# Kernel optimization log

Hardware: AMD Instinct MI355X
Metric: run time of the kernel (lower is better)

The kernel has to match this reference:

```python
import jax, jax.numpy as jnp
import numpy as np

B, N, H, S, NSEC = 1, 8192, 256, 128, 8
TAU = 0.5
DEPTH_LO, DEPTH_HI = 0.0, 2.4
PADDING = 0.1
EPS = 1e-6
_p = float(np.clip(TAU, 1e-4, 1.0 - 1e-4))
LOGIT_TAU = float(np.log(_p / (1.0 - _p)))


def mlp(p, W1, b1, W2, b2, W3, b3, W4, b4):
    # p: [..., 3] -> logit [...]
    h = jax.nn.softplus(p @ W1 + b1)
    h = jax.nn.softplus(h @ W2 + b2)
    h = jax.nn.softplus(h @ W3 + b3)
    return (h @ W4 + b4)[..., 0]


def cube_intersection(ray0, rd):
    # Faithful port of check_ray_intersection_with_unit_cube.
    p_dist = 0.5 + PADDING / 2.0
    plane = jnp.concatenate([jnp.full((3,), p_dist), jnp.full((3,), -p_dist)])  # (6,)
    nom = plane - jnp.tile(ray0, (1, 1, 2))          # (B,N,6)
    den = jnp.tile(rd, (1, 1, 2))
    den = jnp.where(jnp.abs(den) < 1e-9, 1e-9, den)  # numerical guard
    d_int = nom / den                                 # (B,N,6)
    p_int = ray0[:, :, None, :] + d_int[..., None] * rd[:, :, None, :]  # (B,N,6,3)
    inside = jnp.all(jnp.abs(p_int) <= p_dist + EPS, axis=-1)           # (B,N,6)
    mask = inside.sum(-1) == 2                                           # rays hitting cube
    # pick the (exactly two) intersecting planes in ascending plane order,
    # matching torch boolean indexing semantics
    plane_id = jnp.arange(6)
    key = jnp.where(inside, plane_id, plane_id + 6)
    idx2 = jnp.argsort(key, axis=-1)[..., :2]                            # (B,N,2)
    p2 = jnp.take_along_axis(p_int, idx2[..., None], axis=2)            # (B,N,2,3)
    norm_rd = jnp.linalg.norm(rd, axis=-1)                               # (B,N)
    d2 = jnp.linalg.norm(p2 - ray0[:, :, None, :], axis=-1) / norm_rd[..., None]
    d2 = jnp.where(mask[..., None], d2, 0.0)
    d2 = jnp.sort(d2, axis=-1)
    return d2, mask


def _secant(d_low, f_low, d_high, f_high):
    den = f_high - f_low
    den = jnp.where(jnp.abs(den) < 1e-12, 1e-12, den)
    return -f_low * (d_high - d_low) / den + d_low


def reference(ray0, ray_direction, W1, b1, W2, b2, W3, b3, W4, b4):
    rd = ray_direction
    dec = lambda p: mlp(p, W1, b1, W2, b2, W3, b3, W4, b4)
    sg = jax.lax.stop_gradient

    # ---- proposal depths (no grad, as torch no_grad ray-marching) ----
    t = jnp.linspace(0.0, 1.0, S)                       # (S,)
    d_default = DEPTH_LO + t * (DEPTH_HI - DEPTH_LO)
    d2, mask_cube = cube_intersection(ray0, rd)
    d_cube = d2[..., 0:1] + t * (d2[..., 1:2] - d2[..., 0:1])   # (B,N,S)
    d_prop = jnp.where(mask_cube[..., None], d_cube, d_default)
    d_prop = sg(d_prop)

    p_prop = sg(ray0)[:, :, None, :] + d_prop[..., None] * sg(rd)[:, :, None, :]
    val = sg(dec(p_prop)) - LOGIT_TAU                   # (B,N,S)

    mask_0_not_occupied = val[..., 0] < 0
    sign_matrix = jnp.concatenate(
        [jnp.sign(val[..., :-1] * val[..., 1:]), jnp.ones(val.shape[:-1] + (1,), val.dtype)], -1)
    cost = sign_matrix * jnp.arange(S, 0, -1, dtype=val.dtype)
    idx = jnp.argmin(cost, -1)                          # first sign-change step
    vmin = jnp.min(cost, -1)
    f_low = jnp.take_along_axis(val, idx[..., None], -1)[..., 0]
    mask = (vmin < 0) & (f_low < 0) & mask_0_not_occupied

    idx_hi = jnp.minimum(idx + 1, S - 1)
    d_low = jnp.take_along_axis(d_prop, idx[..., None], -1)[..., 0]
    d_high = jnp.take_along_axis(d_prop, idx_hi[..., None], -1)[..., 0]
    f_high = jnp.take_along_axis(val, idx_hi[..., None], -1)[..., 0]

    # ---- secant refinement (no grad in torch) ----
    r0s, rds = sg(ray0), sg(rd)
    d_pred = _secant(d_low, f_low, d_high, f_high)
    for _ in range(NSEC):
        f_mid = sg(dec(r0s + d_pred[..., None] * rds)) - LOGIT_TAU
        low = f_mid < 0
        d_low = jnp.where(low, d_pred, d_low)
        f_low = jnp.where(low, f_mid, f_low)
        d_high = jnp.where(low, d_high, d_pred)
        f_high = jnp.where(low, f_high, f_mid)
        d_pred = _secant(d_low, f_low, d_high, f_high)

    # ---- differentiable implicit-gradient correction (analytic backward of
    # DepthFunction: dd/dtheta = -(df/dtheta)/(df/dd) at the surface point) ----
    d_star = sg(d_pred)
    f_of_d = lambda d: dec(ray0 + d[..., None] * rd) - LOGIT_TAU
    f_val = f_of_d(d_star)                              # differentiable wrt params/rays
    _, df_dd = jax.jvp(f_of_d, (d_star,), (jnp.ones_like(d_star),))
    df_dd = sg(df_dd)
    df_dd = jnp.where(jnp.abs(df_dd) < 1e-6,
                      jnp.where(df_dd < 0, -1e-6, 1e-6), df_dd)
    d_out = d_star - f_val / df_dd
    d_final = jnp.where(mask, d_out, 0.0)
    return d_final


def setup_inputs() -> dict:
    key = jax.random.key(0)
    ks = jax.random.split(key, 10)
    origin = jnp.array([0.0, 0.0, -1.5])
    ray0 = origin + 0.01 * jax.random.normal(ks[0], (B, N, 3), dtype=jnp.float32)
    target = jax.random.uniform(ks[1], (B, N, 3), minval=-0.4, maxval=0.4, dtype=jnp.float32)
    rd = target - ray0
    rd = rd / jnp.linalg.norm(rd, axis=-1, keepdims=True)
    W1 = jax.random.normal(ks[2], (3, H), dtype=jnp.float32) / jnp.sqrt(3.0)
    b1 = 0.1 * jax.random.normal(ks[3], (H,), dtype=jnp.float32)
    W2 = jax.random.normal(ks[4], (H, H), dtype=jnp.float32) / jnp.sqrt(float(H))
    b2 = 0.1 * jax.random.normal(ks[5], (H,), dtype=jnp.float32)
    W3 = jax.random.normal(ks[6], (H, H), dtype=jnp.float32) / jnp.sqrt(float(H))
    b3 = 0.1 * jax.random.normal(ks[7], (H,), dtype=jnp.float32)
    W4 = jax.random.normal(ks[8], (H, 1), dtype=jnp.float32) / jnp.sqrt(float(H))
    b4 = 0.1 * jax.random.normal(ks[9], (1,), dtype=jnp.float32)
    return {"ray0": ray0, "ray_direction": rd, "W1": W1, "b1": b1,
            "W2": W2, "b2": b2, "W3": W3, "b3": b3, "W4": W4, "b4": b4}
```

## Files before the change

kernel.cpp:

```cpp
#include <hip/hip_runtime.h>
#include <math.h>

#define NRAY 8192
#define SSAMP 128
#define HD 256
#define AROW 264
#define A1ROW 40
#define FIXCAP 262144
#define FIXTHR 0.025f

typedef short s16x8 __attribute__((ext_vector_type(8)));
typedef float f32x4 __attribute__((ext_vector_type(4)));

__device__ __forceinline__ unsigned short f2bf(float f) {
    unsigned u = __float_as_uint(f);
    u += 0x7fffu + ((u >> 16) & 1u);
    return (unsigned short)(u >> 16);
}
__device__ __forceinline__ unsigned short f2bf_t(float f) {
    return (unsigned short)(__float_as_uint(f) >> 16);
}
__device__ __forceinline__ float bf2f(unsigned short s) {
    return __uint_as_float(((unsigned)s) << 16);
}
__device__ __forceinline__ void split2(float f, unsigned short& hi, unsigned short& lo) {
    unsigned u = __float_as_uint(f);
    hi = (unsigned short)(u >> 16);
    float r = f - __uint_as_float(u & 0xFFFF0000u);
    lo = f2bf(r);
}
__device__ __forceinline__ float softplus_fast(float x) {
    return fmaxf(x, 0.0f) + __logf(1.0f + __expf(-fabsf(x)));
}
__device__ __forceinline__ float softplus_cheap(float x) {
    float m = __expf(-fabsf(x));
    float p = fmaf(m, fmaf(0.14258f, m, -0.44943f), 1.0f);
    return fmaxf(x, 0.0f) + m * p;
}
__device__ __forceinline__ float sigmoid_fast(float x) {
    return 1.0f / (1.0f + __expf(-x));
}

__global__ __launch_bounds__(256)
void prep_kernel(const float* __restrict__ W1, const float* __restrict__ b1,
                 const float* __restrict__ W2, const float* __restrict__ W3,
                 const float* __restrict__ ray0, const float* __restrict__ rdg,
                 unsigned short* __restrict__ P2, unsigned short* __restrict__ P3,
                 unsigned short* __restrict__ B1, float* __restrict__ rayinfo,
                 int* __restrict__ fix_cnt) {
    const int b = blockIdx.x, tid = threadIdx.x;
    if (b < 256) {
        int idx = b * 256 + tid;
        int k = idx >> 8, n = idx & 255;
        int nt = n >> 4, kt = k >> 5, lq = (k >> 3) & 3, j = k & 7;
        int lane = (lq << 4) | (n & 15);
        size_t off = (size_t)((nt * 8 + kt) * 2) * 512 + (size_t)lane * 8 + j;
        float w = W2[idx];
        unsigned short hi = f2bf(w);
        P2[off] = hi; P2[off + 512] = f2bf(w - bf2f(hi));
        w = W3[idx];
        hi = f2bf(w);
        P3[off] = hi; P3[off + 512] = f2bf(w - bf2f(hi));
    } else if (b < 288) {
        int idx = (b - 256) * 256 + tid;
        int w = idx & 511;
        int lane = w >> 3, j = w & 7;
        int k = ((lane >> 4) << 3) + j;
        int n = ((idx >> 9) << 4) + (lane & 15);
        unsigned short s = 0;
        if (k < 3) s = f2bf(W1[k * HD + n]);
        else if (k == 3) s = f2bf(b1[n]);
        else if (k < 7) s = f2bf(W1[(k - 4) * HD + n]);
        else if (k == 7) { unsigned short bh = f2bf(b1[n]); s = f2bf(b1[n] - bf2f(bh)); }
        else if (k < 11) { float wv = W1[(k - 8) * HD + n]; unsigned short wh = f2bf(wv); s = f2bf(wv - bf2f(wh)); }
        B1[idx] = s;
    } else {
        int r = (b - 288) * 256 + tid;
        if (r == 0) *fix_cnt = 0;
        float o0 = ray0[3 * r], o1 = ray0[3 * r + 1], o2 = ray0[3 * r + 2];
        float v0 = rdg[3 * r], v1 = rdg[3 * r + 1], v2 = rdg[3 * r + 2];
        const float pd = 0.55f, lim = pd + 1e-6f;
        float di[6]; int insk[6]; int cnt = 0;
        for (int k = 0; k < 6; k++) {
            int a = k % 3;
            float pl = (k < 3) ? pd : -pd;
            float den = (a == 0) ? v0 : ((a == 1) ? v1 : v2);
            if (fabsf(den) < 1e-9f) den = 1e-9f;
            float oa = (a == 0) ? o0 : ((a == 1) ? o1 : o2);
            float dd = (pl - oa) / den;
            float px = o0 + dd * v0, py = o1 + dd * v1, pz = o2 + dd * v2;
            int ins = (fabsf(px) <= lim) && (fabsf(py) <= lim) && (fabsf(pz) <= lim);
            di[k] = dd; insk[k] = ins; cnt += ins;
        }
        float d0 = 0.f, sl = 2.4f;
        if (cnt == 2) {
            int k1 = -1, k2 = -1;
            for (int k = 0; k < 6; k++) if (insk[k]) { if (k1 < 0) k1 = k; else k2 = k; }
            float nrd = sqrtf(v0 * v0 + v1 * v1 + v2 * v2);
            float ax = di[k1] * v0, ay = di[k1] * v1, az = di[k1] * v2;
            float d1n = sqrtf(ax * ax + ay * ay + az * az) / nrd;
            float bx = di[k2] * v0, by = di[k2] * v1, bz = di[k2] * v2;
            float d2n = sqrtf(bx * bx + by * by + bz * bz) / nrd;
            d0 = fminf(d1n, d2n);
            sl = fmaxf(d1n, d2n) - d0;
        }
        float* ri = rayinfo + (size_t)r * 8;
        ri[0] = d0; ri[1] = sl;
        ri[2] = o0; ri[3] = o1; ri[4] = o2;
        ri[5] = v0; ri[6] = v1; ri[7] = v2;
    }
}

template<int MT>
__device__ __forceinline__ void gemm_l1(const unsigned short* A1,
                                        const unsigned short* __restrict__ B1,
                                        f32x4 acc[MT][4], int lane, int ntbase) {
    const int r15 = lane & 15, q = lane >> 4;
    s16x8 bh[4];
#pragma unroll
    for (int nt = 0; nt < 4; nt++)
        bh[nt] = *(((const s16x8*)B1) + (size_t)(ntbase + nt) * 64 + lane);
#pragma unroll
    for (int mt = 0; mt < MT; mt++) {
        s16x8 ah = *(const s16x8*)(A1 + (mt * 16 + r15) * A1ROW + q * 8);
#pragma unroll
        for (int nt = 0; nt < 4; nt++)
            acc[mt][nt] = __builtin_amdgcn_mfma_f32_16x16x32_bf16(ah, bh[nt], (f32x4){0.f,0.f,0.f,0.f}, 0, 0, 0);
    }
}

template<int MT>
__device__ __forceinline__ void gemm_1t(const unsigned short* Ahi,
                                        const unsigned short* __restrict__ Bp,
                                        f32x4 acc[MT][4], int lane, int ntbase) {
#pragma unroll
    for (int mt = 0; mt < MT; mt++)
#pragma unroll
        for (int nt = 0; nt < 4; nt++) acc[mt][nt] = (f32x4){0.f, 0.f, 0.f, 0.f};
    const int r15 = lane & 15, q = lane >> 4;
#pragma unroll 2
    for (int kt = 0; kt < 8; kt++) {
        s16x8 bh[4];
#pragma unroll
        for (int nt = 0; nt < 4; nt++) {
            const s16x8* bp = ((const s16x8*)Bp) + (size_t)((ntbase + nt) * 8 + kt) * 128 + lane;
            bh[nt] = bp[0];
        }
        const int kc = kt * 32 + q * 8;
#pragma unroll
        for (int mt = 0; mt < MT; mt++) {
            s16x8 ah = *(const s16x8*)(Ahi + (mt * 16 + r15) * AROW + kc);
#pragma unroll
            for (int nt = 0; nt < 4; nt++)
                acc[mt][nt] = __builtin_amdgcn_mfma_f32_16x16x32_bf16(ah, bh[nt], acc[mt][nt], 0, 0, 0);
        }
    }
}

template<int MT>
__device__ __forceinline__ void gemm_3t(const unsigned short* Ahi, const unsigned short* Alo,
                                        const unsigned short* __restrict__ Bp,
                                        f32x4 acc[MT][4], int lane, int ntbase) {
#pragma unroll
    for (int mt = 0; mt < MT; mt++)
#pragma unroll
        for (int nt = 0; nt < 4; nt++) acc[mt][nt] = (f32x4){0.f, 0.f, 0.f, 0.f};
    const int r15 = lane & 15, q = lane >> 4;
#pragma unroll 2
    for (int kt = 0; kt < 8; kt++) {
        s16x8 bh[4], bl[4];
#pragma unroll
        for (int nt = 0; nt < 4; nt++) {
            const s16x8* bp = ((const s16x8*)Bp) + (size_t)((ntbase + nt) * 8 + kt) * 128 + lane;
            bh[nt] = bp[0];
            bl[nt] = bp[64];
        }
        const int kc = kt * 32 + q * 8;
#pragma unroll
        for (int mt = 0; mt < MT; mt++) {
            s16x8 ah = *(const s16x8*)(Ahi + (mt * 16 + r15) * AROW + kc);
            s16x8 al = *(const s16x8*)(Alo + (mt * 16 + r15) * AROW + kc);
#pragma unroll
            for (int nt = 0; nt < 4; nt++) {
                acc[mt][nt] = __builtin_amdgcn_mfma_f32_16x16x32_bf16(ah, bh[nt], acc[mt][nt], 0, 0, 0);
                acc[mt][nt] = __builtin_amdgcn_mfma_f32_16x16x32_bf16(ah, bl[nt], acc[mt][nt], 0, 0, 0);
                acc[mt][nt] = __builtin_amdgcn_mfma_f32_16x16x32_bf16(al, bh[nt], acc[mt][nt], 0, 0, 0);
            }
        }
    }
}

template<int MT>
__device__ __forceinline__ void gemm_dual(const unsigned short* Avh, const unsigned short* Avl,
                                          const unsigned short* Ath, const unsigned short* Atl,
                                          const unsigned short* __restrict__ Bp,
                                          f32x4 av[MT][4], f32x4 at[MT][4], int lane, int ntbase) {
#pragma unroll
    for (int mt = 0; mt < MT; mt++)
#pragma unroll
        for (int nt = 0; nt < 4; nt++) {
            av[mt][nt] = (f32x4){0.f, 0.f, 0.f, 0.f};
            at[mt][nt] = (f32x4){0.f, 0.f, 0.f, 0.f};
        }
    const int r15 = lane & 15, q = lane >> 4;
#pragma unroll 2
    for (int kt = 0; kt < 8; kt++) {
        s16x8 bh[4], bl[4];
#pragma unroll
        for (int nt = 0; nt < 4; nt++) {
            const s16x8* bp = ((const s16x8*)Bp) + (size_t)((ntbase + nt) * 8 + kt) * 128 + lane;
            bh[nt] = bp[0];
            bl[nt] = bp[64];
        }
        const int kc = kt * 32 + q * 8;
#pragma unroll
        for (int mt = 0; mt < MT; mt++) {
            s16x8 avh = *(const s16x8*)(Avh + (mt * 16 + r15) * AROW + kc);
            s16x8 avl = *(const s16x8*)(Avl + (mt * 16 + r15) * AROW + kc);
            s16x8 ath = *(const s16x8*)(Ath + (mt * 16 + r15) * AROW + kc);
            s16x8 atl = *(const s16x8*)(Atl + (mt * 16 + r15) * AROW + kc);
#pragma unroll
            for (int nt = 0; nt < 4; nt++) {
                av[mt][nt] = __builtin_amdgcn_mfma_f32_16x16x32_bf16(avh, bh[nt], av[mt][nt], 0, 0, 0);
                av[mt][nt] = __builtin_amdgcn_mfma_f32_16x16x32_bf16(avh, bl[nt], av[mt][nt], 0, 0, 0);
                av[mt][nt] = __builtin_amdgcn_mfma_f32_16x16x32_bf16(avl, bh[nt], av[mt][nt], 0, 0, 0);
                at[mt][nt] = __builtin_amdgcn_mfma_f32_16x16x32_bf16(ath, bh[nt], at[mt][nt], 0, 0, 0);
                at[mt][nt] = __builtin_amdgcn_mfma_f32_16x16x32_bf16(ath, bl[nt], at[mt][nt], 0, 0, 0);
                at[mt][nt] = __builtin_amdgcn_mfma_f32_16x16x32_bf16(atl, bh[nt], at[mt][nt], 0, 0, 0);
            }
        }
    }
}

template<int MT>
__device__ __forceinline__ void epi_l1(f32x4 acc[MT][4], unsigned short* Ahi, int lane, int wn0) {
    const int r15 = lane & 15, q = lane >> 4;
#pragma unroll
    for (int mt = 0; mt < MT; mt++)
#pragma unroll
        for (int nt = 0; nt < 4; nt++) {
            int col = wn0 + nt * 16 + r15;
#pragma unroll
            for (int reg = 0; reg < 4; reg++) {
                int row = mt * 16 + q * 4 + reg;
                Ahi[row * AROW + col] = f2bf_t(softplus_cheap(acc[mt][nt][reg]));
            }
        }
}

template<int MT>
__device__ __forceinline__ void epi_l1_sp(f32x4 acc[MT][4], unsigned short* Ahi, unsigned short* Alo,
                                          int lane, int wn0) {
    const int r15 = lane & 15, q = lane >> 4;
#pragma unroll
    for (int mt = 0; mt < MT; mt++)
#pragma unroll
        for (int nt = 0; nt < 4; nt++) {
            int col = wn0 + nt * 16 + r15;
#pragma unroll
            for (int reg = 0; reg < 4; reg++) {
                int row = mt * 16 + q * 4 + reg;
                float h = softplus_fast(acc[mt][nt][reg]);
                unsigned short hi, lo;
                split2(h, hi, lo);
                Ahi[row * AROW + col] = hi;
                Alo[row * AROW + col] = lo;
            }
        }
}

template<int MT>
__device__ __forceinline__ void epi_hidden_1t(f32x4 acc[MT][4], const float* __restrict__ b,
                                              unsigned short* Ahi, int lane, int wn0) {
    const int r15 = lane & 15, q = lane >> 4;
#pragma unroll
    for (int mt = 0; mt < MT; mt++)
#pragma unroll
        for (int nt = 0; nt < 4; nt++) {
            int col = wn0 + nt * 16 + r15;
            float bb = b[col];
#pragma unroll
            for (int reg = 0; reg < 4; reg++) {
                int row = mt * 16 + q * 4 + reg;
                Ahi[row * AROW + col] = f2bf_t(softplus_cheap(acc[mt][nt][reg] + bb));
            }
        }
}

template<int MT>
__device__ __forceinline__ void epi_hidden_sp(f32x4 acc[MT][4], const float* __restrict__ b,
                                              unsigned short* Ahi, unsigned short* Alo,
                                              int lane, int wn0) {
    const int r15 = lane & 15, q = lane >> 4;
#pragma unroll
    for (int mt = 0; mt < MT; mt++)
#pragma unroll
        for (int nt = 0; nt < 4; nt++) {
            int col = wn0 + nt * 16 + r15;
            float bb = b[col];
#pragma unroll
            for (int reg = 0; reg < 4; reg++) {
                int row = mt * 16 + q * 4 + reg;
                float h = softplus_fast(acc[mt][nt][reg] + bb);
                unsigned short hi, lo;
                split2(h, hi, lo);
                Ahi[row * AROW + col] = hi;
                Alo[row * AROW + col] = lo;
            }
        }
}

template<int MT>
__device__ __forceinline__ void epi_dual(f32x4 av[MT][4], f32x4 at[MT][4], const float* __restrict__ b,
                                         unsigned short* Avh, unsigned short* Avl,
                                         unsigned short* Ath, unsigned short* Atl,
                                         int lane, int wn0) {
    const int r15 = lane & 15, q = lane >> 4;
#pragma unroll
    for (int mt = 0; mt < MT; mt++)
#pragma unroll
        for (int nt = 0; nt < 4; nt++) {
            int col = wn0 + nt * 16 + r15;
            float bb = b[col];
#pragma unroll
            for (int reg = 0; reg < 4; reg++) {
                int row = mt * 16 + q * 4 + reg;
                float z = av[mt][nt][reg] + bb;
                float h = softplus_fast(z);
                float ht = sigmoid_fast(z) * at[mt][nt][reg];
                unsigned short hi, lo;
                split2(h, hi, lo);
                Avh[row * AROW + col] = hi;
                Avl[row * AROW + col] = lo;
                split2(ht, hi, lo);
                Ath[row * AROW + col] = hi;
                Atl[row * AROW + col] = lo;
            }
        }
}

template<int MT, bool CH>
__device__ __forceinline__ void l4_reduce(f32x4 acc[MT][4], const float* __restrict__ b3,
                                          const float* __restrict__ W4,
                                          float* partial, int lane, int wn0) {
    const int r15 = lane & 15, q = lane >> 4;
    float w4v[4], b3v[4];
#pragma unroll
    for (int nt = 0; nt < 4; nt++) {
        int col = wn0 + nt * 16 + r15;
        w4v[nt] = W4[col]; b3v[nt] = b3[col];
    }
#pragma unroll
    for (int mt = 0; mt < MT; mt++)
#pragma unroll
        for (int reg = 0; reg < 4; reg++) {
            float p = 0.f;
#pragma unroll
            for (int nt = 0; nt < 4; nt++) {
                float z = acc[mt][nt][reg] + b3v[nt];
                float h = CH ? softplus_cheap(z) : softplus_fast(z);
                p += h * w4v[nt];
            }
#pragma unroll
            for (int m = 1; m < 16; m <<= 1) p += __shfl_xor(p, m, 64);
            if (r15 == 0) partial[mt * 16 + q * 4 + reg] = p;
        }
}

template<int MT>
__device__ __forceinline__ void l4_reduce_dual(f32x4 av[MT][4], f32x4 at[MT][4],
                                               const float* __restrict__ b3, const float* __restrict__ W4,
                                               float* pv, float* pt, int lane, int wn0) {
    const int r15 = lane & 15, q = lane >> 4;
    float w4v[4], b3v[4];
#pragma unroll
    for (int nt = 0; nt < 4; nt++) {
        int col = wn0 + nt * 16 + r15;
        w4v[nt] = W4[col]; b3v[nt] = b3[col];
    }
#pragma unroll
    for (int mt = 0; mt < MT; mt++)
#pragma unroll
        for (int reg = 0; reg < 4; reg++) {
            float sv = 0.f, st = 0.f;
#pragma unroll
            for (int nt = 0; nt < 4; nt++) {
                float z = av[mt][nt][reg] + b3v[nt];
                sv += softplus_fast(z) * w4v[nt];
                st += sigmoid_fast(z) * at[mt][nt][reg] * w4v[nt];
            }
#pragma unroll
            for (int m = 1; m < 16; m <<= 1) {
                sv += __shfl_xor(sv, m, 64);
                st += __shfl_xor(st, m, 64);
            }
            if (r15 == 0) {
                pv[mt * 16 + q * 4 + reg] = sv;
                pt[mt * 16 + q * 4 + reg] = st;
            }
        }
}

__global__ __launch_bounds__(256, 4)
void coarse_mfma(const float* __restrict__ rayinfo,
                 const unsigned short* __restrict__ B1,
                 const unsigned short* __restrict__ P2, const float* __restrict__ b2,
                 const unsigned short* __restrict__ P3, const float* __restrict__ b3,
                 const float* __restrict__ W4, const float* __restrict__ b4,
                 float* __restrict__ val_out, float* __restrict__ dprop_out,
                 int* __restrict__ fix_cnt, int* __restrict__ fix_list) {
    __shared__ __align__(16) unsigned short Ahi[64 * AROW];
    __shared__ __align__(16) unsigned short A1[64 * A1ROW];
    float* partial = (float*)A1;
    const int tid = threadIdx.x;
    const int lane = tid & 63, wave = tid >> 6;
    const int r = blockIdx.x >> 1, half = blockIdx.x & 1;

    if (tid < 64) {
        const float* ri = rayinfo + (size_t)r * 8;
        const int s = half * 64 + tid;
        float t = (float)s * (1.0f / 127.0f);
        float d = fmaf(t, ri[1], ri[0]);
        dprop_out[r * SSAMP + s] = d;
        float px = fmaf(d, ri[5], ri[2]);
        float py = fmaf(d, ri[6], ri[3]);
        float pz = fmaf(d, ri[7], ri[4]);
        unsigned short hx, lx, hy, ly, hz, lz;
        split2(px, hx, lx); split2(py, hy, ly); split2(pz, hz, lz);
        unsigned short* row = A1 + tid * A1ROW;
        row[0] = hx; row[1] = hy; row[2] = hz; row[3] = 0x3F80u;
        row[4] = lx; row[5] = ly; row[6] = lz; row[7] = 0x3F80u;
        row[8] = hx; row[9] = hy; row[10] = hz;
#pragma unroll
        for (int c = 11; c < 32; c++) row[c] = 0;
    }
    __syncthreads();
    f32x4 acc[4][4];
    gemm_l1<4>(A1, B1, acc, lane, wave * 4);
    epi_l1<4>(acc, Ahi, lane, wave * 64);
    __syncthreads();
    gemm_1t<4>(Ahi, P2, acc, lane, wave * 4);
    __syncthreads();
    epi_hidden_1t<4>(acc, b2, Ahi, lane, wave * 64);
    __syncthreads();
    gemm_1t<4>(Ahi, P3, acc, lane, wave * 4);
    l4_reduce<4, true>(acc, b3, W4, &partial[wave * 64], lane, wave * 64);
    __syncthreads();
    if (tid < 64) {
        float v = partial[tid] + partial[64 + tid] + partial[128 + tid] + partial[192 + tid] + b4[0];
        int idx = r * SSAMP + half * 64 + tid;
        val_out[idx] = v;
        if (fabsf(v) < FIXTHR) {
            int pos = atomicAdd(fix_cnt, 1);
            if (pos < FIXCAP) fix_list[pos] = idx;
        }
    }
}

__global__ __launch_bounds__(256, 2)
void fixup3_mfma(const int* __restrict__ counter, const int* __restrict__ list,
                 float* __restrict__ val, const float* __restrict__ dprop,
                 const float* __restrict__ ray0, const float* __restrict__ rdg,
                 const unsigned short* __restrict__ B1,
                 const unsigned short* __restrict__ P2, const float* __restrict__ b2,
                 const unsigned short* __restrict__ P3, const float* __restrict__ b3,
                 const float* __restrict__ W4, const float* __restrict__ b4) {
    __shared__ __align__(16) unsigned short Ahi[64 * AROW];
    __shared__ __align__(16) unsigned short Alo[64 * AROW];
    __shared__ __align__(16) unsigned short A1[64 * A1ROW];
    __shared__ float partial[4][64];
    __shared__ int bidxs[64];
    const int cnt = min(*counter, FIXCAP);
    const int base = blockIdx.x * 64;
    if (base >= cnt) return;
    const int tid = threadIdx.x;
    const int lane = tid & 63, wave = tid >> 6;
    if (tid < 64) {
        const int i = min(base + tid, cnt - 1);
        const int bidx = list[i];
        bidxs[tid] = bidx;
        const int rr = bidx >> 7;
        float d = dprop[bidx];
        float px = ray0[3 * rr] + d * rdg[3 * rr];
        float py = ray0[3 * rr + 1] + d * rdg[3 * rr + 1];
        float pz = ray0[3 * rr + 2] + d * rdg[3 * rr + 2];
        unsigned short hx, lx, hy, ly, hz, lz;
        split2(px, hx, lx); split2(py, hy, ly); split2(pz, hz, lz);
        unsigned short* row = A1 + tid * A1ROW;
        row[0] = hx; row[1] = hy; row[2] = hz; row[3] = 0x3F80u;
        row[4] = lx; row[5] = ly; row[6] = lz; row[7] = 0x3F80u;
        row[8] = hx; row[9] = hy; row[10] = hz;
#pragma unroll
        for (int c = 11; c < 32; c++) row[c] = 0;
    }
    __syncthreads();
    f32x4 acc[4][4];
    gemm_l1<4>(A1, B1, acc, lane, wave * 4);
    epi_l1_sp<4>(acc, Ahi, Alo, lane, wave * 64);
    __syncthreads();
    gemm_3t<4>(Ahi, Alo, P2, acc, lane, wave * 4);
    __syncthreads();
    epi_hidden_sp<4>(acc, b2, Ahi, Alo, lane, wave * 64);
    __syncthreads();
    gemm_3t<4>(Ahi, Alo, P3, acc, lane, wave * 4);
    l4_reduce<4, false>(acc, b3, W4, &partial[wave][0], lane, wave * 64);
    __syncthreads();
    if (tid < 64) {
        float v = partial[0][tid] + partial[1][tid] + partial[2][tid] + partial[3][tid] + b4[0];
        val[bidxs[tid]] = v;
    }
}

__global__ __launch_bounds__(256, 4)
void refine_mfma(const float* __restrict__ val, const float* __restrict__ dprop,
                 const float* __restrict__ ray0, const float* __restrict__ rdg,
                 const float* __restrict__ W1, const float* __restrict__ b1,
                 const unsigned short* __restrict__ P2, const float* __restrict__ b2,
                 const unsigned short* __restrict__ P3, const float* __restrict__ b3,
                 const float* __restrict__ W4, const float* __restrict__ b4,
                 float* __restrict__ out) {
    __shared__ __align__(16) unsigned short Avh[16 * AROW];
    __shared__ __align__(16) unsigned short Avl[16 * AROW];
    __shared__ __align__(16) unsigned short Ath[16 * AROW];
    __shared__ __align__(16) unsigned short Atl[16 * AROW];
    __shared__ float partial[4][16], ptan[4][16];
    __shared__ float dl[16], fl[16], dh[16], fh[16], dps[16];
    __shared__ int mks[16];
    unsigned short* Ahi = Avh;
    const int tid = threadIdx.x;
    const int lane = tid & 63, wave = tid >> 6;
    const int r0 = blockIdx.x * 16;

    for (int i = 0; i < 4; i++) {
        const int r = r0 + wave * 4 + i;
        const float2 v = *(const float2*)(val + (size_t)r * SSAMP + lane * 2);
        const float2 dd = *(const float2*)(dprop + (size_t)r * SSAMP + lane * 2);
        float vnext = __shfl_down(v.x, 1, 64);
        const int s0 = lane * 2, s1 = s0 + 1;
        float pr0 = v.x * v.y;
        int sg0 = (pr0 > 0.f) ? 1 : ((pr0 < 0.f) ? -1 : 0);
        int k0 = (sg0 * (SSAMP - s0) + 129) * 256 + s0;
        int k1;
        if (lane == 63) {
            k1 = (1 + 129) * 256 + 127;
        } else {
            float pr1 = v.y * vnext;
            int sg1 = (pr1 > 0.f) ? 1 : ((pr1 < 0.f) ? -1 : 0);
            k1 = (sg1 * (SSAMP - s1) + 129) * 256 + s1;
        }
        int k = min(k0, k1);
#pragma unroll
        for (int m = 1; m < 64; m <<= 1) k = min(k, __shfl_xor(k, m, 64));
        int bidx = k & 255;
        int cmin = (k >> 8) - 129;
        int idxh = min(bidx + 1, SSAMP - 1);
        int ow = bidx >> 1, oh = idxh >> 1;
        float fa = __shfl(v.x, ow, 64), fb = __shfl(v.y, ow, 64);
        float da = __shfl(dd.x, ow, 64), db = __shfl(dd.y, ow, 64);
        float fa2 = __shfl(v.x, oh, 64), fb2 = __shfl(v.y, oh, 64);
        float da2 = __shfl(dd.x, oh, 64), db2 = __shfl(dd.y, oh, 64);
        float v0 = __shfl(v.x, 0, 64);
        if (lane == 0) {
            float f_low = (bidx & 1) ? fb : fa;
            float d_low = (bidx & 1) ? db : da;
            float f_high = (idxh & 1) ? fb2 : fa2;
            float d_high = (idxh & 1) ? db2 : da2;
            int sl = wave * 4 + i;
            mks[sl] = (cmin < 0) && (f_low < 0.f) && (v0 < 0.f);
            float den = f_high - f_low;
            if (fabsf(den) < 1e-12f) den = 1e-12f;
            dl[sl] = d_low; fl[sl] = f_low; dh[sl] = d_high; fh[sl] = f_high;
            dps[sl] = -f_low * (d_high - d_low) / den + d_low;
        }
    }
    __syncthreads();
    for (int it = 0; it < 8; it++) {
        {
            const int pt = tid >> 4, jb = (tid & 15) << 4;
            const int rr = r0 + pt;
            float d = dps[pt];
            float px = ray0[3 * rr] + d * rdg[3 * rr];
            float py = ray0[3 * rr + 1] + d * rdg[3 * rr + 1];
            float pz = ray0[3 * rr + 2] + d * rdg[3 * rr + 2];
            for (int j = jb; j < jb + 16; j += 4) {
                float4 wa = *(const float4*)(W1 + j);
                float4 wb = *(const float4*)(W1 + 256 + j);
                float4 wc = *(const float4*)(W1 + 512 + j);
                float4 bb = *(const float4*)(b1 + j);
                float z[4];
                z[0] = fmaf(px, wa.x, fmaf(py, wb.x, fmaf(pz, wc.x, bb.x)));
                z[1] = fmaf(px, wa.y, fmaf(py, wb.y, fmaf(pz, wc.y, bb.y)));
                z[2] = fmaf(px, wa.z, fmaf(py, wb.z, fmaf(pz, wc.z, bb.z)));
                z[3] = fmaf(px, wa.w, fmaf(py, wb.w, fmaf(pz, wc.w, bb.w)));
#pragma unroll
                for (int i = 0; i < 4; i++)
                    Ahi[pt * AROW + j + i] = f2bf_t(softplus_cheap(z[i]));
            }
        }
        __syncthreads();
        f32x4 acc[1][4];
        gemm_1t<1>(Ahi, P2, acc, lane, wave * 4);
        __syncthreads();
        epi_hidden_1t<1>(acc, b2, Ahi, lane, wave * 64);
        __syncthreads();
        gemm_1t<1>(Ahi, P3, acc, lane, wave * 4);
        l4_reduce<1, true>(acc, b3, W4, &partial[wave][0], lane, wave * 64);
        __syncthreads();
        if (tid < 16) {
            float fm = partial[0][tid] + partial[1][tid] + partial[2][tid] + partial[3][tid] + b4[0];
            float dpv = dps[tid];
            float dlv = dl[tid], flv = fl[tid], dhv = dh[tid], fhv = fh[tid];
            if (fm < 0.f) { dlv = dpv; flv = fm; } else { dhv = dpv; fhv = fm; }
            float den = fhv - flv;
            if (fabsf(den) < 1e-12f) den = 1e-12f;
            dps[tid] = -flv * (dhv - dlv) / den + dlv;
            dl[tid] = dlv; fl[tid] = flv; dh[tid] = dhv; fh[tid] = fhv;
        }
        __syncthreads();
    }
    {
        const int pt = tid >> 4, jb = (tid & 15) << 4;
        const int rr = r0 + pt;
        float d = dps[pt];
        float v0 = rdg[3 * rr], v1 = rdg[3 * rr + 1], v2 = rdg[3 * rr + 2];
        float px = ray0[3 * rr] + d * v0;
        float py = ray0[3 * rr + 1] + d * v1;
        float pz = ray0[3 * rr + 2] + d * v2;
        for (int j = jb; j < jb + 16; j += 4) {
            float4 wa = *(const float4*)(W1 + j);
            float4 wb = *(const float4*)(W1 + 256 + j);
            float4 wc = *(const float4*)(W1 + 512 + j);
            float4 bb = *(const float4*)(b1 + j);
            float z[4], zt[4];
            z[0] = fmaf(px, wa.x, fmaf(py, wb.x, fmaf(pz, wc.x, bb.x)));
            z[1] = fmaf(px, wa.y, fmaf(py, wb.y, fmaf(pz, wc.y, bb.y)));
            z[2] = fmaf(px, wa.z, fmaf(py, wb.z, fmaf(pz, wc.z, bb.z)));
            z[3] = fmaf(px, wa.w, fmaf(py, wb.w, fmaf(pz, wc.w, bb.w)));
            zt[0] = fmaf(v0, wa.x, fmaf(v1, wb.x, v2 * wc.x));
            zt[1] = fmaf(v0, wa.y, fmaf(v1, wb.y, v2 * wc.y));
            zt[2] = fmaf(v0, wa.z, fmaf(v1, wb.z, v2 * wc.z));
            zt[3] = fmaf(v0, wa.w, fmaf(v1, wb.w, v2 * wc.w));
#pragma unroll
            for (int i = 0; i < 4; i++) {
                float h = softplus_fast(z[i]);
                float ht = sigmoid_fast(z[i]) * zt[i];
                unsigned short hi, lo;
                split2(h, hi, lo);
                Avh[pt * AROW + j + i] = hi;
                Avl[pt * AROW + j + i] = lo;
                split2(ht, hi, lo);
                Ath[pt * AROW + j + i] = hi;
                Atl[pt * AROW + j + i] = lo;
            }
        }
    }
    __syncthreads();
    f32x4 av[1][4], at[1][4];
    gemm_dual<1>(Avh, Avl, Ath, Atl, P2, av, at, lane, wave * 4);
    __syncthreads();
    epi_dual<1>(av, at, b2, Avh, Avl, Ath, Atl, lane, wave * 64);
    __syncthreads();
    gemm_dual<1>(Avh, Avl, Ath, Atl, P3, av, at, lane, wave * 4);
    l4_reduce_dual<1>(av, at, b3, W4, &partial[wave][0], &ptan[wave][0], lane, wave * 64);
    __syncthreads();
    if (tid < 16) {
        float f = partial[0][tid] + partial[1][tid] + partial[2][tid] + partial[3][tid] + b4[0];
        float ft = ptan[0][tid] + ptan[1][tid] + ptan[2][tid] + ptan[3][tid];
        if (fabsf(ft) < 1e-6f) ft = (ft < 0.f) ? -1e-6f : 1e-6f;
        float dres = dps[tid] - f / ft;
        out[r0 + tid] = mks[tid] ? dres : 0.0f;
    }
}

extern "C" void kernel_launch(void* const* d_in, const int* in_sizes, int n_in,
                              void* d_out, int out_size, void* d_ws, size_t ws_size,
                              hipStream_t stream) {
    const float* ray0 = (const float*)d_in[0];
    const float* rdg  = (const float*)d_in[1];
    const float* W1 = (const float*)d_in[2];
    const float* b1 = (const float*)d_in[3];
    const float* W2 = (const float*)d_in[4];
    const float* b2 = (const float*)d_in[5];
    const float* W3 = (const float*)d_in[6];
    const float* b3 = (const float*)d_in[7];
    const float* W4 = (const float*)d_in[8];
    const float* b4 = (const float*)d_in[9];
    float* out = (float*)d_out;

    float* ws = (float*)d_ws;
    float* val    = ws;
    float* dprop  = ws + (size_t)SSAMP * NRAY;
    unsigned short* P2 = (unsigned short*)(ws + (size_t)2 * SSAMP * NRAY);
    unsigned short* P3 = P2 + 131072;
    unsigned short* B1 = P3 + 131072;
    float* rayinfo = (float*)(B1 + 8192);
    int* fix_cnt  = (int*)(rayinfo + (size_t)NRAY * 8);
    int* fix_list = fix_cnt + 64;

    hipLaunchKernelGGL(prep_kernel, dim3(320), dim3(256), 0, stream,
                       W1, b1, W2, W3, ray0, rdg, P2, P3, B1, rayinfo, fix_cnt);
    hipLaunchKernelGGL(coarse_mfma, dim3(NRAY * 2), dim3(256), 0, stream,
                       rayinfo, B1, P2, b2, P3, b3, W4, b4, val, dprop, fix_cnt, fix_list);
    hipLaunchKernelGGL(fixup3_mfma, dim3(FIXCAP / 64), dim3(256), 0, stream,
                       fix_cnt, fix_list, val, dprop, ray0, rdg,
                       B1, P2, b2, P3, b3, W4, b4);
    hipLaunchKernelGGL(refine_mfma, dim3(NRAY / 16), dim3(256), 0, stream,
                       val, dprop, ray0, rdg, W1, b1, P2, b2, P3, b3, W4, b4, out);
}
```

Before: 718.2 us.

## Split refine kernel into 8-ray, 2-wave blocks with wider per-wave N tiles

The refine kernel now handles 8 rays per block with 128 threads instead of 16 rays with 256 threads, which doubles the grid size. Each of the two waves covers 8 output n-tiles, using new gemm, epilogue and reduce helpers sized for 8 tiles. The MFMA M dimension is still 16, so rows 8-15 of the shared tangent and value buffers are zeroed and half of each MFMA does no useful work. The aim is more blocks in flight to hide latency in this small, serial secant/Newton stage, paid for with wasted matrix work and more B-fragment register pressure.

```diff
diff --git a/kernel.cpp b/kernel.cpp
--- a/kernel.cpp
+++ b/kernel.cpp
@@ -191,48 +191,6 @@
 }
 
 template<int MT>
-__device__ __forceinline__ void gemm_dual(const unsigned short* Avh, const unsigned short* Avl,
-                                          const unsigned short* Ath, const unsigned short* Atl,
-                                          const unsigned short* __restrict__ Bp,
-                                          f32x4 av[MT][4], f32x4 at[MT][4], int lane, int ntbase) {
-#pragma unroll
-    for (int mt = 0; mt < MT; mt++)
-#pragma unroll
-        for (int nt = 0; nt < 4; nt++) {
-            av[mt][nt] = (f32x4){0.f, 0.f, 0.f, 0.f};
-            at[mt][nt] = (f32x4){0.f, 0.f, 0.f, 0.f};
-        }
-    const int r15 = lane & 15, q = lane >> 4;
-#pragma unroll 2
-    for (int kt = 0; kt < 8; kt++) {
-        s16x8 bh[4], bl[4];
-#pragma unroll
-        for (int nt = 0; nt < 4; nt++) {
-            const s16x8* bp = ((const s16x8*)Bp) + (size_t)((ntbase + nt) * 8 + kt) * 128 + lane;
-            bh[nt] = bp[0];
-            bl[nt] = bp[64];
-        }
-        const int kc = kt * 32 + q * 8;
-#pragma unroll
-        for (int mt = 0; mt < MT; mt++) {
-            s16x8 avh = *(const s16x8*)(Avh + (mt * 16 + r15) * AROW + kc);
-            s16x8 avl = *(const s16x8*)(Avl + (mt * 16 + r15) * AROW + kc);
-            s16x8 ath = *(const s16x8*)(Ath + (mt * 16 + r15) * AROW + kc);
-            s16x8 atl = *(const s16x8*)(Atl + (mt * 16 + r15) * AROW + kc);
-#pragma unroll
-            for (int nt = 0; nt < 4; nt++) {
-                av[mt][nt] = __builtin_amdgcn_mfma_f32_16x16x32_bf16(avh, bh[nt], av[mt][nt], 0, 0, 0);
-                av[mt][nt] = __builtin_amdgcn_mfma_f32_16x16x32_bf16(avh, bl[nt], av[mt][nt], 0, 0, 0);
-                av[mt][nt] = __builtin_amdgcn_mfma_f32_16x16x32_bf16(avl, bh[nt], av[mt][nt], 0, 0, 0);
-                at[mt][nt] = __builtin_amdgcn_mfma_f32_16x16x32_bf16(ath, bh[nt], at[mt][nt], 0, 0, 0);
-                at[mt][nt] = __builtin_amdgcn_mfma_f32_16x16x32_bf16(ath, bl[nt], at[mt][nt], 0, 0, 0);
-                at[mt][nt] = __builtin_amdgcn_mfma_f32_16x16x32_bf16(atl, bh[nt], at[mt][nt], 0, 0, 0);
-            }
-        }
-    }
-}
-
-template<int MT>
 __device__ __forceinline__ void epi_l1(f32x4 acc[MT][4], unsigned short* Ahi, int lane, int wn0) {
     const int r15 = lane & 15, q = lane >> 4;
 #pragma unroll
@@ -310,35 +268,6 @@
         }
 }
 
-template<int MT>
-__device__ __forceinline__ void epi_dual(f32x4 av[MT][4], f32x4 at[MT][4], const float* __restrict__ b,
-                                         unsigned short* Avh, unsigned short* Avl,
-                                         unsigned short* Ath, unsigned short* Atl,
-                                         int lane, int wn0) {
-    const int r15 = lane & 15, q = lane >> 4;
-#pragma unroll
-    for (int mt = 0; mt < MT; mt++)
-#pragma unroll
-        for (int nt = 0; nt < 4; nt++) {
-            int col = wn0 + nt * 16 + r15;
-            float bb = b[col];
-#pragma unroll
-            for (int reg = 0; reg < 4; reg++) {
-                int row = mt * 16 + q * 4 + reg;
-                float z = av[mt][nt][reg] + bb;
-                float h = softplus_fast(z);
-                float ht = sigmoid_fast(z) * at[mt][nt][reg];
-                unsigned short hi, lo;
-                split2(h, hi, lo);
-                Avh[row * AROW + col] = hi;
-                Avl[row * AROW + col] = lo;
-                split2(ht, hi, lo);
-                Ath[row * AROW + col] = hi;
-                Atl[row * AROW + col] = lo;
-            }
-        }
-}
-
 template<int MT, bool CH>
 __device__ __forceinline__ void l4_reduce(f32x4 acc[MT][4], const float* __restrict__ b3,
                                           const float* __restrict__ W4,
@@ -367,38 +296,153 @@
         }
 }
 
-template<int MT>
-__device__ __forceinline__ void l4_reduce_dual(f32x4 av[MT][4], f32x4 at[MT][4],
-                                               const float* __restrict__ b3, const float* __restrict__ W4,
-                                               float* pv, float* pt, int lane, int wn0) {
-    const int r15 = lane & 15, q = lane >> 4;
-    float w4v[4], b3v[4];
-#pragma unroll
-    for (int nt = 0; nt < 4; nt++) {
+__device__ __forceinline__ void gemm_1t8(const unsigned short* Ahi,
+                                         const unsigned short* __restrict__ Bp,
+                                         f32x4 acc[8], int lane, int ntbase) {
+#pragma unroll
+    for (int nt = 0; nt < 8; nt++) acc[nt] = (f32x4){0.f, 0.f, 0.f, 0.f};
+    const int r15 = lane & 15, q = lane >> 4;
+#pragma unroll 2
+    for (int kt = 0; kt < 8; kt++) {
+        s16x8 bh[8];
+#pragma unroll
+        for (int nt = 0; nt < 8; nt++)
+            bh[nt] = *(((const s16x8*)Bp) + (size_t)((ntbase + nt) * 8 + kt) * 128 + lane);
+        const int kc = kt * 32 + q * 8;
+        s16x8 ah = *(const s16x8*)(Ahi + r15 * AROW + kc);
+#pragma unroll
+        for (int nt = 0; nt < 8; nt++)
+            acc[nt] = __builtin_amdgcn_mfma_f32_16x16x32_bf16(ah, bh[nt], acc[nt], 0, 0, 0);
+    }
+}
+
+__device__ __forceinline__ void gemm_dual8(const unsigned short* Avh, const unsigned short* Avl,
+                                           const unsigned short* Ath, const unsigned short* Atl,
+                                           const unsigned short* __restrict__ Bp,
+                                           f32x4 av[8], f32x4 at[8], int lane, int ntbase) {
+#pragma unroll
+    for (int nt = 0; nt < 8; nt++) {
+        av[nt] = (f32x4){0.f, 0.f, 0.f, 0.f};
+        at[nt] = (f32x4){0.f, 0.f, 0.f, 0.f};
+    }
+    const int r15 = lane & 15, q = lane >> 4;
+    for (int kt = 0; kt < 8; kt++) {
+        const int kc = kt * 32 + q * 8;
+        s16x8 avh = *(const s16x8*)(Avh + r15 * AROW + kc);
+        s16x8 avl = *(const s16x8*)(Avl + r15 * AROW + kc);
+        s16x8 ath = *(const s16x8*)(Ath + r15 * AROW + kc);
+        s16x8 atl = *(const s16x8*)(Atl + r15 * AROW + kc);
+#pragma unroll
+        for (int nt = 0; nt < 8; nt++) {
+            const s16x8* bp = ((const s16x8*)Bp) + (size_t)((ntbase + nt) * 8 + kt) * 128 + lane;
+            s16x8 bh = bp[0];
+            s16x8 bl = bp[64];
+            av[nt] = __builtin_amdgcn_mfma_f32_16x16x32_bf16(avh, bh, av[nt], 0, 0, 0);
+            av[nt] = __builtin_amdgcn_mfma_f32_16x16x32_bf16(avh, bl, av[nt], 0, 0, 0);
+            av[nt] = __builtin_amdgcn_mfma_f32_16x16x32_bf16(avl, bh, av[nt], 0, 0, 0);
+            at[nt] = __builtin_amdgcn_mfma_f32_16x16x32_bf16(ath, bh, at[nt], 0, 0, 0);
+            at[nt] = __builtin_amdgcn_mfma_f32_16x16x32_bf16(ath, bl, at[nt], 0, 0, 0);
+            at[nt] = __builtin_amdgcn_mfma_f32_16x16x32_bf16(atl, bh, at[nt], 0, 0, 0);
+        }
+    }
+}
+
+__device__ __forceinline__ void epi_hidden8(f32x4 acc[8], const float* __restrict__ b,
+                                            unsigned short* Ahi, int lane, int wn0) {
+    const int r15 = lane & 15, q = lane >> 4;
+#pragma unroll
+    for (int nt = 0; nt < 8; nt++) {
+        int col = wn0 + nt * 16 + r15;
+        float bb = b[col];
+#pragma unroll
+        for (int reg = 0; reg < 4; reg++) {
+            int row = q * 4 + reg;
+            Ahi[row * AROW + col] = f2bf_t(softplus_cheap(acc[nt][reg] + bb));
+        }
+    }
+}
+
+__device__ __forceinline__ void epi_dual8(f32x4 av[8], f32x4 at[8], const float* __restrict__ b,
+                                          unsigned short* Avh, unsigned short* Avl,
+                                          unsigned short* Ath, unsigned short* Atl,
+                                          int lane, int wn0) {
+    const int r15 = lane & 15, q = lane >> 4;
+#pragma unroll
+    for (int nt = 0; nt < 8; nt++) {
+        int col = wn0 + nt * 16 + r15;
+        float bb = b[col];
+#pragma unroll
+        for (int reg = 0; reg < 4; reg++) {
+            int row = q * 4 + reg;
+            float z = av[nt][reg] + bb;
+            float h = softplus_fast(z);
+            float ht = sigmoid_fast(z) * at[nt][reg];
+            unsigned short hi, lo;
+            split2(h, hi, lo);
+            Avh[row * AROW + col] = hi;
+            Avl[row * AROW + col] = lo;
+            split2(ht, hi, lo);
+            Ath[row * AROW + col] = hi;
+            Atl[row * AROW + col] = lo;
+        }
+    }
+}
+
+template<bool CH>
+__device__ __forceinline__ void l4_reduce8(f32x4 acc[8], const float* __restrict__ b3,
+                                           const float* __restrict__ W4,
+                                           float* partial, int lane, int wn0) {
+    const int r15 = lane & 15, q = lane >> 4;
+    float w4v[8], b3v[8];
+#pragma unroll
+    for (int nt = 0; nt < 8; nt++) {
         int col = wn0 + nt * 16 + r15;
         w4v[nt] = W4[col]; b3v[nt] = b3[col];
     }
 #pragma unroll
-    for (int mt = 0; mt < MT; mt++)
-#pragma unroll
-        for (int reg = 0; reg < 4; reg++) {
-            float sv = 0.f, st = 0.f;
-#pragma unroll
-            for (int nt = 0; nt < 4; nt++) {
-                float z = av[mt][nt][reg] + b3v[nt];
-                sv += softplus_fast(z) * w4v[nt];
-                st += sigmoid_fast(z) * at[mt][nt][reg] * w4v[nt];
-            }
-#pragma unroll
-            for (int m = 1; m < 16; m <<= 1) {
-                sv += __shfl_xor(sv, m, 64);
-                st += __shfl_xor(st, m, 64);
-            }
-            if (r15 == 0) {
-                pv[mt * 16 + q * 4 + reg] = sv;
-                pt[mt * 16 + q * 4 + reg] = st;
-            }
-        }
+    for (int reg = 0; reg < 4; reg++) {
+        float p = 0.f;
+#pragma unroll
+        for (int nt = 0; nt < 8; nt++) {
+            float z = acc[nt][reg] + b3v[nt];
+            float h = CH ? softplus_cheap(z) : softplus_fast(z);
+            p += h * w4v[nt];
+        }
+#pragma unroll
+        for (int m = 1; m < 16; m <<= 1) p += __shfl_xor(p, m, 64);
+        if (r15 == 0) partial[q * 4 + reg] = p;
+    }
+}
+
+__device__ __forceinline__ void l4_reduce_dual8(f32x4 av[8], f32x4 at[8],
+                                                const float* __restrict__ b3, const float* __restrict__ W4,
+                                                float* pv, float* pt, int lane, int wn0) {
+    const int r15 = lane & 15, q = lane >> 4;
+    float w4v[8], b3v[8];
+#pragma unroll
+    for (int nt = 0; nt < 8; nt++) {
+        int col = wn0 + nt * 16 + r15;
+        w4v[nt] = W4[col]; b3v[nt] = b3[col];
+    }
+#pragma unroll
+    for (int reg = 0; reg < 4; reg++) {
+        float sv = 0.f, st = 0.f;
+#pragma unroll
+        for (int nt = 0; nt < 8; nt++) {
+            float z = av[nt][reg] + b3v[nt];
+            sv += softplus_fast(z) * w4v[nt];
+            st += sigmoid_fast(z) * at[nt][reg] * w4v[nt];
+        }
+#pragma unroll
+        for (int m = 1; m < 16; m <<= 1) {
+            sv += __shfl_xor(sv, m, 64);
+            st += __shfl_xor(st, m, 64);
+        }
+        if (r15 == 0) {
+            pv[q * 4 + reg] = sv;
+            pt[q * 4 + reg] = st;
+        }
+    }
 }
 
 __global__ __launch_bounds__(256, 4)
@@ -511,7 +555,7 @@
     }
 }
 
-__global__ __launch_bounds__(256, 4)
+__global__ __launch_bounds__(128, 2)
 void refine_mfma(const float* __restrict__ val, const float* __restrict__ dprop,
                  const float* __restrict__ ray0, const float* __restrict__ rdg,
                  const float* __restrict__ W1, const float* __restrict__ b1,
@@ -523,13 +567,13 @@
     __shared__ __align__(16) unsigned short Avl[16 * AROW];
     __shared__ __align__(16) unsigned short Ath[16 * AROW];
     __shared__ __align__(16) unsigned short Atl[16 * AROW];
-    __shared__ float partial[4][16], ptan[4][16];
-    __shared__ float dl[16], fl[16], dh[16], fh[16], dps[16];
-    __shared__ int mks[16];
+    __shared__ float partial[2][16], ptan[2][16];
+    __shared__ float dl[8], fl[8], dh[8], fh[8], dps[8];
+    __shared__ int mks[8];
     unsigned short* Ahi = Avh;
     const int tid = threadIdx.x;
     const int lane = tid & 63, wave = tid >> 6;
-    const int r0 = blockIdx.x * 16;
+    const int r0 = blockIdx.x * 8;
 
     for (int i = 0; i < 4; i++) {
         const int r = r0 + wave * 4 + i;
@@ -598,16 +642,16 @@
             }
         }
         __syncthreads();
-        f32x4 acc[1][4];
-        gemm_1t<1>(Ahi, P2, acc, lane, wave * 4);
+        f32x4 acc[8];
+        gemm_1t8(Ahi, P2, acc, lane, wave * 8);
         __syncthreads();
-        epi_hidden_1t<1>(acc, b2, Ahi, lane, wave * 64);
+        epi_hidden8(acc, b2, Ahi, lane, wave * 128);
         __syncthreads();
-        gemm_1t<1>(Ahi, P3, acc, lane, wave * 4);
-        l4_reduce<1, true>(acc, b3, W4, &partial[wave][0], lane, wave * 64);
+        gemm_1t8(Ahi, P3, acc, lane, wave * 8);
+        l4_reduce8<true>(acc, b3, W4, &partial[wave][0], lane, wave * 128);
         __syncthreads();
-        if (tid < 16) {
-            float fm = partial[0][tid] + partial[1][tid] + partial[2][tid] + partial[3][tid] + b4[0];
+        if (tid < 8) {
+            float fm = partial[0][tid] + partial[1][tid] + b4[0];
             float dpv = dps[tid];
             float dlv = dl[tid], flv = fl[tid], dhv = dh[tid], fhv = fh[tid];
             if (fm < 0.f) { dlv = dpv; flv = fm; } else { dhv = dpv; fhv = fm; }
@@ -653,19 +697,27 @@
                 Atl[pt * AROW + j + i] = lo;
             }
         }
-    }
-    __syncthreads();
-    f32x4 av[1][4], at[1][4];
-    gemm_dual<1>(Avh, Avl, Ath, Atl, P2, av, at, lane, wave * 4);
-    __syncthreads();
-    epi_dual<1>(av, at, b2, Avh, Avl, Ath, Atl, lane, wave * 64);
-    __syncthreads();
-    gemm_dual<1>(Avh, Avl, Ath, Atl, P3, av, at, lane, wave * 4);
-    l4_reduce_dual<1>(av, at, b3, W4, &partial[wave][0], &ptan[wave][0], lane, wave * 64);
-    __syncthreads();
-    if (tid < 16) {
-        float f = partial[0][tid] + partial[1][tid] + partial[2][tid] + partial[3][tid] + b4[0];
-        float ft = ptan[0][tid] + ptan[1][tid] + ptan[2][tid] + ptan[3][tid];
+        if (tid < 128) {
+            for (int row = 8 + (tid >> 4); row < 16; row += 8) {
+                for (int j = jb; j < jb + 16; j++) {
+                    Avh[row * AROW + j] = 0; Avl[row * AROW + j] = 0;
+                    Ath[row * AROW + j] = 0; Atl[row * AROW + j] = 0;
+                }
+            }
+        }
+    }
+    __syncthreads();
+    f32x4 av[8], at[8];
+    gemm_dual8(Avh, Avl, Ath, Atl, P2, av, at, lane, wave * 8);
+    __syncthreads();
+    epi_dual8(av, at, b2, Avh, Avl, Ath, Atl, lane, wave * 128);
+    __syncthreads();
+    gemm_dual8(Avh, Avl, Ath, Atl, P3, av, at, lane, wave * 8);
+    l4_reduce_dual8(av, at, b3, W4, &partial[wave][0], &ptan[wave][0], lane, wave * 128);
+    __syncthreads();
+    if (tid < 8) {
+        float f = partial[0][tid] + partial[1][tid] + b4[0];
+        float ft = ptan[0][tid] + ptan[1][tid];
         if (fabsf(ft) < 1e-6f) ft = (ft < 0.f) ? -1e-6f : 1e-6f;
         float dres = dps[tid] - f / ft;
         out[r0 + tid] = mks[tid] ? dres : 0.0f;
@@ -704,6 +756,6 @@
     hipLaunchKernelGGL(fixup3_mfma, dim3(FIXCAP / 64), dim3(256), 0, stream,
                        fix_cnt, fix_list, val, dprop, ray0, rdg,
                        B1, P2, b2, P3, b3, W4, b4);
-    hipLaunchKernelGGL(refine_mfma, dim3(NRAY / 16), dim3(256), 0, stream,
+    hipLaunchKernelGGL(refine_mfma, dim3(NRAY / 8), dim3(128), 0, stream,
                        val, dprop, ray0, rdg, W1, b1, P2, b2, P3, b3, W4, b4, out);
 }
```

Result: no change. 723.1 us (+0.7%).
